# Optimization experiments

Measured on AMD Instinct MI355X. Metric: run time of the kernel, lower is better.

The kernel has to match this reference:

```python
import jax, jax.numpy as jnp
import numpy as np

E = 8        # n_routed_experts
K = 2        # n_experts_per_token
H = 1024     # d_hidden
D = 512      # d_expert
NSH = 2      # n_shared_experts -> shared expert width = D*NSH


def setup_inputs() -> dict:
    key = jax.random.key(0)
    ks = jax.random.split(key, 8)
    s = 0.02
    x = jax.random.normal(ks[0], (4, 2048, H), jnp.float32)
    W_router = (jax.random.normal(ks[1], (H, E), jnp.float32) * s)
    Wg = (jax.random.normal(ks[2], (E, H, D), jnp.float32) * s)   # per-expert gate proj
    Wu = (jax.random.normal(ks[3], (E, H, D), jnp.float32) * s)   # per-expert up proj
    Wd = (jax.random.normal(ks[4], (E, D, H), jnp.float32) * s)   # per-expert down proj
    Ds = D * NSH
    Wsg = (jax.random.normal(ks[5], (H, Ds), jnp.float32) * s)
    Wsu = (jax.random.normal(ks[6], (H, Ds), jnp.float32) * s)
    Wsd = (jax.random.normal(ks[7], (Ds, H), jnp.float32) * s)
    return {"x": x, "W_router": W_router, "Wg": Wg, "Wu": Wu, "Wd": Wd,
            "Wsg": Wsg, "Wsu": Wsu, "Wsd": Wsd}


def reference(x, W_router, Wg, Wu, Wd, Wsg, Wsu, Wsd):
    B, S, Hd = x.shape
    T = B * S
    xf = x.reshape(T, Hd)

    # shared expert (SwiGLU)
    shared = (jax.nn.silu(xf @ Wsg) * (xf @ Wsu)) @ Wsd          # [T, H]

    # gating: softmax -> top-k -> renormalize
    logits = xf @ W_router                                        # [T, E]
    probs = jax.nn.softmax(logits, axis=-1)
    topk_scores, topk_idx = jax.lax.top_k(probs, K)               # [T, K]
    topk_scores = topk_scores / jnp.sum(topk_scores, axis=-1, keepdims=True)

    # combine weights: zero for unselected experts (topk indices are distinct,
    # so the original's first-match score selection equals a simple scatter)
    combine = jnp.zeros((T, E), x.dtype).at[jnp.arange(T)[:, None], topk_idx].set(topk_scores)

    # per-expert SwiGLU, computed densely and combined with sparse weights
    gate = jax.nn.silu(jnp.einsum('th,ehd->etd', xf, Wg))         # [E, T, D]
    up = jnp.einsum('th,ehd->etd', xf, Wu)                        # [E, T, D]
    expert_out = jnp.einsum('etd,edh->eth', gate * up, Wd)        # [E, T, H]
    routed = jnp.einsum('eth,te->th', expert_out, combine)        # [T, H]

    out = (routed + shared).reshape(B, S, Hd)

    # load-balancing aux loss: E * sum(mean_probs^2)
    probs_mean = jnp.mean(probs.reshape(B, S, E), axis=(0, 1))
    aux_loss = E * jnp.sum(probs_mean * probs_mean)
    return out, aux_loss
```

## Files before the change

kernel.cpp:

```cpp
#include <hip/hip_runtime.h>


typedef unsigned short u16;
typedef unsigned int   u32;
typedef short short8 __attribute__((ext_vector_type(8)));
typedef float f32x4  __attribute__((ext_vector_type(4)));

#define AS1 __attribute__((address_space(1)))
#define AS3 __attribute__((address_space(3)))

constexpr int T  = 8192;
constexpr int H  = 1024;
constexpr int E  = 8;
constexpr int D  = 512;
constexpr int DS = 1024;
constexpr int PAIR_CAP  = 17408;
constexpr int MT_ROUTED = 136;
constexpr int RB = 256;

__device__ __forceinline__ u16 f2bf(float f){
  u32 u = __builtin_bit_cast(u32, f);
  u += 0x7fffu + ((u >> 16) & 1u);
  return (u16)(u >> 16);
}
__device__ __forceinline__ float bf2f(u16 h){
  u32 u = ((u32)h) << 16;
  return __builtin_bit_cast(float, u);
}

__device__ __forceinline__ void gl_lds16(const u16* g, u16* l){
  __builtin_amdgcn_global_load_lds((const AS1 void*)g, (AS3 void*)l, 16, 0, 0);
}

template<int ROWS>
__device__ __forceinline__ void stage_tile(const u16* __restrict__ gbase, int ld, int k0,
                                           int rowbase, const int* __restrict__ gather,
                                           u16* lds, int wave, int lane){
  constexpr int ISS = ROWS / 32;
  int lr = lane >> 3, ch = lane & 7;
#pragma unroll
  for (int j = 0; j < ISS; ++j){
    int idx = wave * ISS + j;
    int row = idx * 8 + lr;
    int grow = gather ? gather[rowbase + row] : (rowbase + row);
    const u16* g = gbase + (long)grow * ld + k0 + ch * 8;
    gl_lds16(g, lds + idx * 512);
  }
}

__global__ void __launch_bounds__(256) router_kernel(
    const float* __restrict__ x, const float* __restrict__ Wr,
    int* __restrict__ topk_idx, float* __restrict__ topk_w,
    int* __restrict__ partial_hist, float* __restrict__ partial_probs)
{
  __shared__ int   hist_s[4][8];
  __shared__ float ps_s[4][8];
  int tid = threadIdx.x, lane = tid & 63, wv = tid >> 6;
  int   histl[8] = {0,0,0,0,0,0,0,0};
  float psl[8]   = {0.f,0.f,0.f,0.f,0.f,0.f,0.f,0.f};

  for (int it = 0; it < 8; ++it){
    int t = blockIdx.x * 32 + wv * 8 + it;
    const float4* xr = (const float4*)(x + (long)t * H);
    float acc[8];
#pragma unroll
    for (int e = 0; e < 8; ++e) acc[e] = 0.f;
#pragma unroll
    for (int i = 0; i < 4; ++i){
      float4 xv = xr[i * 64 + lane];
      int h0 = i * 256 + lane * 4;
#pragma unroll
      for (int j = 0; j < 4; ++j){
        float xs = (j == 0) ? xv.x : (j == 1) ? xv.y : (j == 2) ? xv.z : xv.w;
        const float4* wr = (const float4*)(Wr + (long)(h0 + j) * E);
        float4 w0 = wr[0], w1 = wr[1];
        acc[0] += xs * w0.x; acc[1] += xs * w0.y; acc[2] += xs * w0.z; acc[3] += xs * w0.w;
        acc[4] += xs * w1.x; acc[5] += xs * w1.y; acc[6] += xs * w1.z; acc[7] += xs * w1.w;
      }
    }
#pragma unroll
    for (int off = 32; off >= 1; off >>= 1){
#pragma unroll
      for (int e = 0; e < 8; ++e) acc[e] += __shfl_xor(acc[e], off, 64);
    }
    if (lane == 0){
      float m = acc[0];
#pragma unroll
      for (int e = 1; e < 8; ++e) m = fmaxf(m, acc[e]);
      float p[8], s = 0.f;
#pragma unroll
      for (int e = 0; e < 8; ++e){ p[e] = __expf(acc[e] - m); s += p[e]; }
      float inv = 1.f / s;
#pragma unroll
      for (int e = 0; e < 8; ++e) psl[e] += p[e] * inv;
      int i1 = 0; float v1 = p[0];
#pragma unroll
      for (int e = 1; e < 8; ++e) if (p[e] > v1){ v1 = p[e]; i1 = e; }
      int i2 = -1; float v2 = -1.f;
#pragma unroll
      for (int e = 0; e < 8; ++e) if (e != i1 && p[e] > v2){ v2 = p[e]; i2 = e; }
      float rs = 1.f / (v1 + v2);
      topk_idx[2 * t] = i1; topk_idx[2 * t + 1] = i2;
      topk_w[2 * t] = v1 * rs; topk_w[2 * t + 1] = v2 * rs;
      histl[i1]++; histl[i2]++;
    }
  }
  if (lane == 0){
#pragma unroll
    for (int e = 0; e < 8; ++e){ hist_s[wv][e] = histl[e]; ps_s[wv][e] = psl[e]; }
  }
  __syncthreads();
  if (tid < 8){
    int hs = 0; float ps = 0.f;
#pragma unroll
    for (int w = 0; w < 4; ++w){ hs += hist_s[w][tid]; ps += ps_s[w][tid]; }
    partial_hist[blockIdx.x * 8 + tid]  = hs;
    partial_probs[blockIdx.x * 8 + tid] = ps;
  }
}

__global__ void __launch_bounds__(64) scan_kernel(
    const int* __restrict__ partial_hist, const float* __restrict__ partial_probs,
    int* __restrict__ block_offset, float* __restrict__ out_aux)
{
  __shared__ int   csum[8][8];
  __shared__ float cps[8][8];
  __shared__ int   cbase[8][8];
  __shared__ int   base_s[8];
  int tid = threadIdx.x, e = tid & 7, c = tid >> 3;
  int s = 0; float f = 0.f;
  for (int b = c * 32; b < c * 32 + 32; ++b){
    s += partial_hist[b * 8 + e]; f += partial_probs[b * 8 + e];
  }
  csum[c][e] = s; cps[c][e] = f;
  __syncthreads();
  if (tid < 8){
    int tot = 0;
    for (int cc = 0; cc < 8; ++cc){ cbase[cc][tid] = tot; tot += csum[cc][tid]; }
    csum[0][tid] = tot;
  }
  __syncthreads();
  if (tid == 0){
    int off = 0;
    for (int ee = 0; ee < 8; ++ee){ base_s[ee] = off; off += (csum[0][ee] + 127) & ~127; }
    float a = 0.f;
    for (int ee = 0; ee < 8; ++ee){
      float ps = 0.f;
      for (int cc = 0; cc < 8; ++cc) ps += cps[cc][ee];
      float m = ps * (1.f / (float)T);
      a += m * m;
    }
    out_aux[0] = (float)E * a;
  }
  __syncthreads();
  int run = base_s[e] + cbase[c][e];
  for (int b = c * 32; b < c * 32 + 32; ++b){
    block_offset[b * 8 + e] = run;
    run += partial_hist[b * 8 + e];
  }
}

__global__ void __launch_bounds__(64) scatter_kernel(
    const int* __restrict__ topk_idx, const float* __restrict__ topk_w,
    const int* __restrict__ block_offset,
    int* __restrict__ pair_token, int* __restrict__ pair_expert,
    float* __restrict__ pair_score, int* __restrict__ token_pos)
{
  int lane = threadIdx.x, b = blockIdx.x;
  int idx = b * 64 + lane;
  int t = idx >> 1;
  int e = topk_idx[idx];
  float w = topk_w[idx];
  unsigned long long below = lane ? ((1ull << lane) - 1ull) : 0ull;
  int rank = 0, basee = 0;
#pragma unroll
  for (int ee = 0; ee < 8; ++ee){
    unsigned long long m = __ballot(e == ee);
    if (e == ee){ rank = __popcll(m & below); basee = block_offset[b * 8 + ee]; }
  }
  int pos = basee + rank;
  pair_token[pos] = t;
  pair_expert[pos] = e;
  pair_score[pos] = w;
  token_pos[idx] = pos;
}

__global__ void __launch_bounds__(256) convert_x_kernel(const float* __restrict__ src, u16* __restrict__ dst){
  int i = blockIdx.x * 256 + threadIdx.x;
  float4 v = ((const float4*)src)[i];
  u32 lo = (u32)f2bf(v.x) | ((u32)f2bf(v.y) << 16);
  u32 hi = (u32)f2bf(v.z) | ((u32)f2bf(v.w) << 16);
  ((uint2*)dst)[i] = make_uint2(lo, hi);
}

__global__ void __launch_bounds__(256) transpose_kernel(const float* __restrict__ src, u16* __restrict__ dst,
                                                        int R, int C){
  __shared__ float tile[32][33];
  long zoff = (long)blockIdx.z * R * C;
  int tx = threadIdx.x & 31, ty = threadIdx.x >> 5;
  int c = blockIdx.x * 32 + tx;
  int rb = blockIdx.y * 32;
#pragma unroll
  for (int j = 0; j < 4; ++j)
    tile[ty + j * 8][tx] = src[zoff + (long)(rb + ty + j * 8) * C + c];
  __syncthreads();
#pragma unroll
  for (int j = 0; j < 4; ++j){
    int cc = blockIdx.x * 32 + ty + j * 8;
    dst[zoff + (long)cc * R + rb + tx] = f2bf(tile[tx][ty + j * 8]);
  }
}

__global__ void __launch_bounds__(256) gateup_kernel(
    const u16* __restrict__ A, const u16* __restrict__ Bg, const u16* __restrict__ Bu,
    u16* __restrict__ Hout, int N, int K,
    const int* __restrict__ gather, const int* __restrict__ pexp, long bstride)
{
  __shared__ u16 As[128 * 64];
  __shared__ u16 Bgs[64 * 64];
  __shared__ u16 Bus[64 * 64];
  int tid = threadIdx.x, lane = tid & 63, wave = tid >> 6;
  int wy = wave >> 1, wx = wave & 1;
  int m0 = blockIdx.y * 128, n0 = blockIdx.x * 64;
  int e = pexp ? pexp[m0] : 0;
  const u16* bg = Bg + (long)e * bstride;
  const u16* bu = Bu + (long)e * bstride;

  f32x4 accG[4][2], accU[4][2];
#pragma unroll
  for (int i = 0; i < 4; ++i)
#pragma unroll
    for (int j = 0; j < 2; ++j)
#pragma unroll
      for (int r = 0; r < 4; ++r){ accG[i][j][r] = 0.f; accU[i][j][r] = 0.f; }

  for (int k0 = 0; k0 < K; k0 += 64){
    stage_tile<128>(A, K, k0, m0, gather, As, wave, lane);
    stage_tile<64>(bg, K, k0, n0, nullptr, Bgs, wave, lane);
    stage_tile<64>(bu, K, k0, n0, nullptr, Bus, wave, lane);
    __syncthreads();
#pragma unroll
    for (int ks = 0; ks < 2; ++ks){
      int ko = ks * 32 + (lane >> 4) * 8;
      short8 a[4], g2[2], u2[2];
#pragma unroll
      for (int mt = 0; mt < 4; ++mt)
        a[mt] = *(const short8*)(As + (wy * 64 + mt * 16 + (lane & 15)) * 64 + ko);
#pragma unroll
      for (int nt = 0; nt < 2; ++nt){
        g2[nt] = *(const short8*)(Bgs + (wx * 32 + nt * 16 + (lane & 15)) * 64 + ko);
        u2[nt] = *(const short8*)(Bus + (wx * 32 + nt * 16 + (lane & 15)) * 64 + ko);
      }
#pragma unroll
      for (int mt = 0; mt < 4; ++mt)
#pragma unroll
        for (int nt = 0; nt < 2; ++nt){
          accG[mt][nt] = __builtin_amdgcn_mfma_f32_16x16x32_bf16(a[mt], g2[nt], accG[mt][nt], 0, 0, 0);
          accU[mt][nt] = __builtin_amdgcn_mfma_f32_16x16x32_bf16(a[mt], u2[nt], accU[mt][nt], 0, 0, 0);
        }
    }
    __syncthreads();
  }
  int row0 = m0 + wy * 64, col0 = n0 + wx * 32;
#pragma unroll
  for (int mt = 0; mt < 4; ++mt)
#pragma unroll
    for (int nt = 0; nt < 2; ++nt)
#pragma unroll
      for (int r = 0; r < 4; ++r){
        int row = row0 + mt * 16 + (lane >> 4) * 4 + r;
        int col = col0 + nt * 16 + (lane & 15);
        float g = accG[mt][nt][r], u = accU[mt][nt][r];
        float h = g / (1.f + __expf(-g)) * u;
        Hout[(long)row * N + col] = f2bf(h);
      }
}

__global__ void __launch_bounds__(256) down_routed_kernel(
    const u16* __restrict__ A, const u16* __restrict__ B, u16* __restrict__ rout,
    const float* __restrict__ pair_score, const int* __restrict__ pexp)
{
  __shared__ u16 As[128 * 64];
  __shared__ u16 Bs[128 * 64];
  int tid = threadIdx.x, lane = tid & 63, wave = tid >> 6;
  int wy = wave >> 1, wx = wave & 1;
  int m0 = blockIdx.y * 128, n0 = blockIdx.x * 128;
  int e = pexp[m0];
  const u16* b = B + (long)e * (H * D);

  f32x4 acc[4][4];
#pragma unroll
  for (int i = 0; i < 4; ++i)
#pragma unroll
    for (int j = 0; j < 4; ++j)
#pragma unroll
      for (int r = 0; r < 4; ++r) acc[i][j][r] = 0.f;

  for (int k0 = 0; k0 < D; k0 += 64){
    stage_tile<128>(A, D, k0, m0, nullptr, As, wave, lane);
    stage_tile<128>(b, D, k0, n0, nullptr, Bs, wave, lane);
    __syncthreads();
#pragma unroll
    for (int ks = 0; ks < 2; ++ks){
      int ko = ks * 32 + (lane >> 4) * 8;
      short8 a[4], bv[4];
#pragma unroll
      for (int mt = 0; mt < 4; ++mt)
        a[mt] = *(const short8*)(As + (wy * 64 + mt * 16 + (lane & 15)) * 64 + ko);
#pragma unroll
      for (int nt = 0; nt < 4; ++nt)
        bv[nt] = *(const short8*)(Bs + (wx * 64 + nt * 16 + (lane & 15)) * 64 + ko);
#pragma unroll
      for (int mt = 0; mt < 4; ++mt)
#pragma unroll
        for (int nt = 0; nt < 4; ++nt)
          acc[mt][nt] = __builtin_amdgcn_mfma_f32_16x16x32_bf16(a[mt], bv[nt], acc[mt][nt], 0, 0, 0);
    }
    __syncthreads();
  }
#pragma unroll
  for (int mt = 0; mt < 4; ++mt)
#pragma unroll
    for (int r = 0; r < 4; ++r){
      int row = m0 + wy * 64 + mt * 16 + (lane >> 4) * 4 + r;
      float s = pair_score[row];
      long rbase = (long)row * H;
#pragma unroll
      for (int nt = 0; nt < 4; ++nt){
        int col = n0 + wx * 64 + nt * 16 + (lane & 15);
        rout[rbase + col] = f2bf(s * acc[mt][nt][r]);
      }
    }
}

__global__ void __launch_bounds__(256) down_shared_kernel(
    const u16* __restrict__ A, const u16* __restrict__ B,
    const u16* __restrict__ rout, const int* __restrict__ token_pos,
    float* __restrict__ out)
{
  __shared__ u16 As[128 * 64];
  __shared__ u16 Bs[128 * 64];
  int tid = threadIdx.x, lane = tid & 63, wave = tid >> 6;
  int wy = wave >> 1, wx = wave & 1;
  int m0 = blockIdx.y * 128, n0 = blockIdx.x * 128;

  f32x4 acc[4][4];
#pragma unroll
  for (int i = 0; i < 4; ++i)
#pragma unroll
    for (int j = 0; j < 4; ++j)
#pragma unroll
      for (int r = 0; r < 4; ++r) acc[i][j][r] = 0.f;

  for (int k0 = 0; k0 < DS; k0 += 64){
    stage_tile<128>(A, DS, k0, m0, nullptr, As, wave, lane);
    stage_tile<128>(B, DS, k0, n0, nullptr, Bs, wave, lane);
    __syncthreads();
#pragma unroll
    for (int ks = 0; ks < 2; ++ks){
      int ko = ks * 32 + (lane >> 4) * 8;
      short8 a[4], bv[4];
#pragma unroll
      for (int mt = 0; mt < 4; ++mt)
        a[mt] = *(const short8*)(As + (wy * 64 + mt * 16 + (lane & 15)) * 64 + ko);
#pragma unroll
      for (int nt = 0; nt < 4; ++nt)
        bv[nt] = *(const short8*)(Bs + (wx * 64 + nt * 16 + (lane & 15)) * 64 + ko);
#pragma unroll
      for (int mt = 0; mt < 4; ++mt)
#pragma unroll
        for (int nt = 0; nt < 4; ++nt)
          acc[mt][nt] = __builtin_amdgcn_mfma_f32_16x16x32_bf16(a[mt], bv[nt], acc[mt][nt], 0, 0, 0);
    }
    __syncthreads();
  }
#pragma unroll
  for (int mt = 0; mt < 4; ++mt)
#pragma unroll
    for (int r = 0; r < 4; ++r){
      int row = m0 + wy * 64 + mt * 16 + (lane >> 4) * 4 + r;
      int p0 = token_pos[2 * row], p1 = token_pos[2 * row + 1];
      long o = (long)row * H;
#pragma unroll
      for (int nt = 0; nt < 4; ++nt){
        int col = n0 + wx * 64 + nt * 16 + (lane & 15);
        out[o + col] = acc[mt][nt][r]
                     + bf2f(rout[(long)p0 * H + col])
                     + bf2f(rout[(long)p1 * H + col]);
      }
    }
}

extern "C" void kernel_launch(void* const* d_in, const int* in_sizes, int n_in,
                              void* d_out, int out_size, void* d_ws, size_t ws_size,
                              hipStream_t stream)
{
  (void)in_sizes; (void)n_in; (void)out_size; (void)ws_size;
  const float* x   = (const float*)d_in[0];
  const float* Wr  = (const float*)d_in[1];
  const float* Wg  = (const float*)d_in[2];
  const float* Wu  = (const float*)d_in[3];
  const float* Wd  = (const float*)d_in[4];
  const float* Wsg = (const float*)d_in[5];
  const float* Wsu = (const float*)d_in[6];
  const float* Wsd = (const float*)d_in[7];
  float* out = (float*)d_out;

  char* ws = (char*)d_ws;
  size_t off = 0;
  auto alloc = [&](size_t bytes) -> void* {
    void* p = ws + off; off += (bytes + 255) & ~(size_t)255; return p;
  };
  u16* xb   = (u16*)alloc((size_t)T * H * 2);
  u16* WsgT = (u16*)alloc((size_t)DS * H * 2);
  u16* WsuT = (u16*)alloc((size_t)DS * H * 2);
  u16* WsdT = (u16*)alloc((size_t)H * DS * 2);
  u16* WgT  = (u16*)alloc((size_t)E * D * H * 2);
  u16* WuT  = (u16*)alloc((size_t)E * D * H * 2);
  u16* WdT  = (u16*)alloc((size_t)E * H * D * 2);
  u16* hs   = (u16*)alloc((size_t)T * DS * 2);
  u16* hr   = (u16*)alloc((size_t)PAIR_CAP * D * 2);
  u16* rout = (u16*)alloc((size_t)PAIR_CAP * H * 2);
  int*   topk_idx  = (int*)alloc((size_t)T * 2 * 4);
  float* topk_w    = (float*)alloc((size_t)T * 2 * 4);
  int*   token_pos = (int*)alloc((size_t)T * 2 * 4);
  int*   partial_hist  = (int*)alloc((size_t)RB * 8 * 4);
  float* partial_probs = (float*)alloc((size_t)RB * 8 * 4);
  int*   block_offset  = (int*)alloc((size_t)RB * 8 * 4);
  char* zbase = ws + off;
  int*   pair_token  = (int*)alloc((size_t)PAIR_CAP * 4);
  int*   pair_expert = (int*)alloc((size_t)PAIR_CAP * 4);
  float* pair_score  = (float*)alloc((size_t)PAIR_CAP * 4);
  size_t zbytes = (size_t)((ws + off) - zbase);

  hipMemsetAsync(zbase, 0, zbytes, stream);

  convert_x_kernel<<<T * H / 4 / 256, 256, 0, stream>>>(x, xb);
  transpose_kernel<<<dim3(DS / 32, H / 32, 1), 256, 0, stream>>>(Wsg, WsgT, H, DS);
  transpose_kernel<<<dim3(DS / 32, H / 32, 1), 256, 0, stream>>>(Wsu, WsuT, H, DS);
  transpose_kernel<<<dim3(H / 32, DS / 32, 1), 256, 0, stream>>>(Wsd, WsdT, DS, H);
  transpose_kernel<<<dim3(D / 32, H / 32, E), 256, 0, stream>>>(Wg, WgT, H, D);
  transpose_kernel<<<dim3(D / 32, H / 32, E), 256, 0, stream>>>(Wu, WuT, H, D);
  transpose_kernel<<<dim3(H / 32, D / 32, E), 256, 0, stream>>>(Wd, WdT, D, H);

  router_kernel<<<RB, 256, 0, stream>>>(x, Wr, topk_idx, topk_w, partial_hist, partial_probs);
  scan_kernel<<<1, 64, 0, stream>>>(partial_hist, partial_probs, block_offset,
                                    out + (size_t)T * H);
  scatter_kernel<<<RB, 64, 0, stream>>>(topk_idx, topk_w, block_offset,
                                        pair_token, pair_expert, pair_score, token_pos);

  gateup_kernel<<<dim3(DS / 64, T / 128), 256, 0, stream>>>(
      xb, WsgT, WsuT, hs, DS, H, nullptr, nullptr, 0);
  gateup_kernel<<<dim3(D / 64, MT_ROUTED), 256, 0, stream>>>(
      xb, WgT, WuT, hr, D, H, pair_token, pair_expert, (long)D * H);
  down_routed_kernel<<<dim3(H / 128, MT_ROUTED), 256, 0, stream>>>(
      hr, WdT, rout, pair_score, pair_expert);
  down_shared_kernel<<<dim3(H / 128, T / 128), 256, 0, stream>>>(
      hs, WsdT, rout, token_pos, out);
}
```

Baseline: 387.4 us.

## Swizzle LDS tiles, fuse x conversion into router, batch transpose launches

```diff
diff --git a/kernel.cpp b/kernel.cpp
--- a/kernel.cpp
+++ b/kernel.cpp
@@ -38,18 +38,24 @@
                                            u16* lds, int wave, int lane){
   constexpr int ISS = ROWS / 32;
   int lr = lane >> 3, ch = lane & 7;
+  int chs = (ch ^ lr) * 8;
 #pragma unroll
   for (int j = 0; j < ISS; ++j){
     int idx = wave * ISS + j;
     int row = idx * 8 + lr;
     int grow = gather ? gather[rowbase + row] : (rowbase + row);
-    const u16* g = gbase + (long)grow * ld + k0 + ch * 8;
+    const u16* g = gbase + (long)grow * ld + k0 + chs;
     gl_lds16(g, lds + idx * 512);
   }
+}
+
+__device__ __forceinline__ int swz_off(int c, int lane){
+  return ((c ^ (lane & 7)) * 8);
 }
 
 __global__ void __launch_bounds__(256) router_kernel(
     const float* __restrict__ x, const float* __restrict__ Wr,
+    u16* __restrict__ xb,
     int* __restrict__ topk_idx, float* __restrict__ topk_w,
     int* __restrict__ partial_hist, float* __restrict__ partial_probs)
 {
@@ -62,12 +68,16 @@
   for (int it = 0; it < 8; ++it){
     int t = blockIdx.x * 32 + wv * 8 + it;
     const float4* xr = (const float4*)(x + (long)t * H);
+    uint2* xbr = (uint2*)(xb + (long)t * H);
     float acc[8];
 #pragma unroll
     for (int e = 0; e < 8; ++e) acc[e] = 0.f;
 #pragma unroll
     for (int i = 0; i < 4; ++i){
       float4 xv = xr[i * 64 + lane];
+      u32 lo = (u32)f2bf(xv.x) | ((u32)f2bf(xv.y) << 16);
+      u32 hi = (u32)f2bf(xv.z) | ((u32)f2bf(xv.w) << 16);
+      xbr[i * 64 + lane] = make_uint2(lo, hi);
       int h0 = i * 256 + lane * 4;
 #pragma unroll
       for (int j = 0; j < 4; ++j){
@@ -185,18 +195,10 @@
   token_pos[idx] = pos;
 }
 
-__global__ void __launch_bounds__(256) convert_x_kernel(const float* __restrict__ src, u16* __restrict__ dst){
-  int i = blockIdx.x * 256 + threadIdx.x;
-  float4 v = ((const float4*)src)[i];
-  u32 lo = (u32)f2bf(v.x) | ((u32)f2bf(v.y) << 16);
-  u32 hi = (u32)f2bf(v.z) | ((u32)f2bf(v.w) << 16);
-  ((uint2*)dst)[i] = make_uint2(lo, hi);
-}
-
-__global__ void __launch_bounds__(256) transpose_kernel(const float* __restrict__ src, u16* __restrict__ dst,
-                                                        int R, int C){
+__device__ __forceinline__ void transpose_body(const float* src, u16* dst, int R, int C,
+                                               int bz){
   __shared__ float tile[32][33];
-  long zoff = (long)blockIdx.z * R * C;
+  long zoff = (long)bz * R * C;
   int tx = threadIdx.x & 31, ty = threadIdx.x >> 5;
   int c = blockIdx.x * 32 + tx;
   int rb = blockIdx.y * 32;
@@ -209,6 +211,29 @@
     int cc = blockIdx.x * 32 + ty + j * 8;
     dst[zoff + (long)cc * R + rb + tx] = f2bf(tile[tx][ty + j * 8]);
   }
+}
+
+__global__ void __launch_bounds__(256) transpose_kernel(const float* __restrict__ src,
+                                                        u16* __restrict__ dst, int R, int C){
+  transpose_body(src, dst, R, C, blockIdx.z);
+}
+
+__global__ void __launch_bounds__(256) transpose2_kernel(
+    const float* __restrict__ s0, u16* __restrict__ d0,
+    const float* __restrict__ s1, u16* __restrict__ d1, int R, int C, int Z){
+  int z = blockIdx.z;
+  if (z < Z) transpose_body(s0, d0, R, C, z);
+  else       transpose_body(s1, d1, R, C, z - Z);
+}
+
+__global__ void __launch_bounds__(256) transpose3_kernel(
+    const float* __restrict__ s0, u16* __restrict__ d0,
+    const float* __restrict__ s1, u16* __restrict__ d1,
+    const float* __restrict__ s2, u16* __restrict__ d2, int R, int C){
+  int z = blockIdx.z;
+  const float* s = (z == 0) ? s0 : (z == 1) ? s1 : s2;
+  u16* d = (z == 0) ? d0 : (z == 1) ? d1 : d2;
+  transpose_body(s, d, R, C, 0);
 }
 
 __global__ void __launch_bounds__(256) gateup_kernel(
@@ -225,6 +250,7 @@
   int e = pexp ? pexp[m0] : 0;
   const u16* bg = Bg + (long)e * bstride;
   const u16* bu = Bu + (long)e * bstride;
+  int rl = lane & 15, q = lane >> 4;
 
   f32x4 accG[4][2], accU[4][2];
 #pragma unroll
@@ -241,15 +267,15 @@
     __syncthreads();
 #pragma unroll
     for (int ks = 0; ks < 2; ++ks){
-      int ko = ks * 32 + (lane >> 4) * 8;
+      int off = swz_off(ks * 4 + q, lane);
       short8 a[4], g2[2], u2[2];
 #pragma unroll
       for (int mt = 0; mt < 4; ++mt)
-        a[mt] = *(const short8*)(As + (wy * 64 + mt * 16 + (lane & 15)) * 64 + ko);
+        a[mt] = *(const short8*)(As + (wy * 64 + mt * 16 + rl) * 64 + off);
 #pragma unroll
       for (int nt = 0; nt < 2; ++nt){
-        g2[nt] = *(const short8*)(Bgs + (wx * 32 + nt * 16 + (lane & 15)) * 64 + ko);
-        u2[nt] = *(const short8*)(Bus + (wx * 32 + nt * 16 + (lane & 15)) * 64 + ko);
+        g2[nt] = *(const short8*)(Bgs + (wx * 32 + nt * 16 + rl) * 64 + off);
+        u2[nt] = *(const short8*)(Bus + (wx * 32 + nt * 16 + rl) * 64 + off);
       }
 #pragma unroll
       for (int mt = 0; mt < 4; ++mt)
@@ -268,8 +294,8 @@
     for (int nt = 0; nt < 2; ++nt)
 #pragma unroll
       for (int r = 0; r < 4; ++r){
-        int row = row0 + mt * 16 + (lane >> 4) * 4 + r;
-        int col = col0 + nt * 16 + (lane & 15);
+        int row = row0 + mt * 16 + q * 4 + r;
+        int col = col0 + nt * 16 + rl;
         float g = accG[mt][nt][r], u = accU[mt][nt][r];
         float h = g / (1.f + __expf(-g)) * u;
         Hout[(long)row * N + col] = f2bf(h);
@@ -287,6 +313,7 @@
   int m0 = blockIdx.y * 128, n0 = blockIdx.x * 128;
   int e = pexp[m0];
   const u16* b = B + (long)e * (H * D);
+  int rl = lane & 15, q = lane >> 4;
 
   f32x4 acc[4][4];
 #pragma unroll
@@ -302,14 +329,14 @@
     __syncthreads();
 #pragma unroll
     for (int ks = 0; ks < 2; ++ks){
-      int ko = ks * 32 + (lane >> 4) * 8;
+      int off = swz_off(ks * 4 + q, lane);
       short8 a[4], bv[4];
 #pragma unroll
       for (int mt = 0; mt < 4; ++mt)
-        a[mt] = *(const short8*)(As + (wy * 64 + mt * 16 + (lane & 15)) * 64 + ko);
+        a[mt] = *(const short8*)(As + (wy * 64 + mt * 16 + rl) * 64 + off);
 #pragma unroll
       for (int nt = 0; nt < 4; ++nt)
-        bv[nt] = *(const short8*)(Bs + (wx * 64 + nt * 16 + (lane & 15)) * 64 + ko);
+        bv[nt] = *(const short8*)(Bs + (wx * 64 + nt * 16 + rl) * 64 + off);
 #pragma unroll
       for (int mt = 0; mt < 4; ++mt)
 #pragma unroll
@@ -322,12 +349,12 @@
   for (int mt = 0; mt < 4; ++mt)
 #pragma unroll
     for (int r = 0; r < 4; ++r){
-      int row = m0 + wy * 64 + mt * 16 + (lane >> 4) * 4 + r;
+      int row = m0 + wy * 64 + mt * 16 + q * 4 + r;
       float s = pair_score[row];
       long rbase = (long)row * H;
 #pragma unroll
       for (int nt = 0; nt < 4; ++nt){
-        int col = n0 + wx * 64 + nt * 16 + (lane & 15);
+        int col = n0 + wx * 64 + nt * 16 + rl;
         rout[rbase + col] = f2bf(s * acc[mt][nt][r]);
       }
     }
@@ -343,6 +370,7 @@
   int tid = threadIdx.x, lane = tid & 63, wave = tid >> 6;
   int wy = wave >> 1, wx = wave & 1;
   int m0 = blockIdx.y * 128, n0 = blockIdx.x * 128;
+  int rl = lane & 15, q = lane >> 4;
 
   f32x4 acc[4][4];
 #pragma unroll
@@ -358,14 +386,14 @@
     __syncthreads();
 #pragma unroll
     for (int ks = 0; ks < 2; ++ks){
-      int ko = ks * 32 + (lane >> 4) * 8;
+      int off = swz_off(ks * 4 + q, lane);
       short8 a[4], bv[4];
 #pragma unroll
       for (int mt = 0; mt < 4; ++mt)
-        a[mt] = *(const short8*)(As + (wy * 64 + mt * 16 + (lane & 15)) * 64 + ko);
+        a[mt] = *(const short8*)(As + (wy * 64 + mt * 16 + rl) * 64 + off);
 #pragma unroll
       for (int nt = 0; nt < 4; ++nt)
-        bv[nt] = *(const short8*)(Bs + (wx * 64 + nt * 16 + (lane & 15)) * 64 + ko);
+        bv[nt] = *(const short8*)(Bs + (wx * 64 + nt * 16 + rl) * 64 + off);
 #pragma unroll
       for (int mt = 0; mt < 4; ++mt)
 #pragma unroll
@@ -378,12 +406,12 @@
   for (int mt = 0; mt < 4; ++mt)
 #pragma unroll
     for (int r = 0; r < 4; ++r){
-      int row = m0 + wy * 64 + mt * 16 + (lane >> 4) * 4 + r;
+      int row = m0 + wy * 64 + mt * 16 + q * 4 + r;
       int p0 = token_pos[2 * row], p1 = token_pos[2 * row + 1];
       long o = (long)row * H;
 #pragma unroll
       for (int nt = 0; nt < 4; ++nt){
-        int col = n0 + wx * 64 + nt * 16 + (lane & 15);
+        int col = n0 + wx * 64 + nt * 16 + rl;
         out[o + col] = acc[mt][nt][r]
                      + bf2f(rout[(long)p0 * H + col])
                      + bf2f(rout[(long)p1 * H + col]);
@@ -435,15 +463,14 @@
 
   hipMemsetAsync(zbase, 0, zbytes, stream);
 
-  convert_x_kernel<<<T * H / 4 / 256, 256, 0, stream>>>(x, xb);
-  transpose_kernel<<<dim3(DS / 32, H / 32, 1), 256, 0, stream>>>(Wsg, WsgT, H, DS);
-  transpose_kernel<<<dim3(DS / 32, H / 32, 1), 256, 0, stream>>>(Wsu, WsuT, H, DS);
-  transpose_kernel<<<dim3(H / 32, DS / 32, 1), 256, 0, stream>>>(Wsd, WsdT, DS, H);
-  transpose_kernel<<<dim3(D / 32, H / 32, E), 256, 0, stream>>>(Wg, WgT, H, D);
-  transpose_kernel<<<dim3(D / 32, H / 32, E), 256, 0, stream>>>(Wu, WuT, H, D);
+  transpose3_kernel<<<dim3(32, 32, 3), 256, 0, stream>>>(
+      Wsg, WsgT, Wsu, WsuT, Wsd, WsdT, 1024, 1024);
+  transpose2_kernel<<<dim3(D / 32, H / 32, 2 * E), 256, 0, stream>>>(
+      Wg, WgT, Wu, WuT, H, D, E);
   transpose_kernel<<<dim3(H / 32, D / 32, E), 256, 0, stream>>>(Wd, WdT, D, H);
 
-  router_kernel<<<RB, 256, 0, stream>>>(x, Wr, topk_idx, topk_w, partial_hist, partial_probs);
+  router_kernel<<<RB, 256, 0, stream>>>(x, Wr, xb, topk_idx, topk_w,
+                                        partial_hist, partial_probs);
   scan_kernel<<<1, 64, 0, stream>>>(partial_hist, partial_probs, block_offset,
                                     out + (size_t)T * H);
   scatter_kernel<<<RB, 64, 0, stream>>>(topk_idx, topk_w, block_offset,
```

Result: faster. 352.5 us (-9.0%).
